# Performance work log

Hardware: AMD Instinct MI355X
Metric: run time of the kernel (lower is better)

## Reference

```python
import jax, jax.numpy as jnp
import numpy as np

D = 1024
H = 16
T_BLOCK = 2048


def setup_inputs() -> dict:
    key = jax.random.key(0)
    ks = jax.random.split(key, 12)
    B, T = 2, 2048
    s = lambda k, shape: jax.random.normal(k, shape, jnp.float32) * 0.02
    return {
        "x": jax.random.normal(ks[0], (B, T, D), jnp.float32),
        # layernorms
        "ln1_g": jnp.ones((D,), jnp.float32), "ln1_b": jnp.zeros((D,), jnp.float32),
        "ln2_g": jnp.ones((D,), jnp.float32), "ln2_b": jnp.zeros((D,), jnp.float32),
        # attention qkv projection ([in,out] layout) and output proj
        "w_qkv": s(ks[1], (D, 3 * D)), "b_qkv": jnp.zeros((3 * D,), jnp.float32),
        "w_o": s(ks[2], (D, D)), "b_o": jnp.zeros((D,), jnp.float32),
        # MLP
        "w_fc1": s(ks[3], (D, 4 * D)), "b_fc1": jnp.zeros((4 * D,), jnp.float32),
        "w_fc2": s(ks[4], (4 * D, D)), "b_fc2": jnp.zeros((D,), jnp.float32),
    }


def _layernorm(x, g, b, eps=1e-5):
    mu = jnp.mean(x, axis=-1, keepdims=True)
    var = jnp.var(x, axis=-1, keepdims=True)
    return (x - mu) * jax.lax.rsqrt(var + eps) * g + b


def _attention(x, w_qkv, b_qkv, w_o, b_o):
    B, T, C = x.shape
    hd = C // H
    qkv = x @ w_qkv + b_qkv                      # [B,T,3C]
    q, k, v = jnp.split(qkv, 3, axis=-1)
    split = lambda t: t.reshape(B, T, H, hd).transpose(0, 2, 1, 3)  # [B,H,T,hd]
    q, k, v = split(q), split(k), split(v)
    att = jnp.einsum("bhqd,bhkd->bhqk", q, k) / jnp.sqrt(jnp.float32(hd))
    causal = jnp.tril(jnp.ones((T, T), bool))
    att = jnp.where(causal[None, None], att, -jnp.inf)
    att = jax.nn.softmax(att, axis=-1)
    y = jnp.einsum("bhqk,bhkd->bhqd", att, v)    # [B,H,T,hd]
    y = y.transpose(0, 2, 1, 3).reshape(B, T, C)
    return y @ w_o + b_o


def reference(x, ln1_g, ln1_b, ln2_g, ln2_b, w_qkv, b_qkv, w_o, b_o,
              w_fc1, b_fc1, w_fc2, b_fc2):
    # dropout is identity in eval mode
    x = x + _attention(_layernorm(x, ln1_g, ln1_b), w_qkv, b_qkv, w_o, b_o)
    h = jax.nn.gelu(_layernorm(x, ln2_g, ln2_b) @ w_fc1 + b_fc1)
    return x + (h @ w_fc2 + b_fc2)
```

## Files before the change

kernel.cpp:

```cpp
#include <hip/hip_runtime.h>
#include <hip/hip_bf16.h>


using bf16 = __bf16;
using bf16x8 = __attribute__((ext_vector_type(8))) __bf16;
using floatx4 = __attribute__((ext_vector_type(4))) float;

#define D_ 1024
#define T_ 2048
#define B_ 2
#define H_ 16

static __device__ __forceinline__ bf16 f2bf(float f) { return (bf16)f; }

static __device__ __forceinline__ void async16(const void* g, void* l) {
  __builtin_amdgcn_global_load_lds(
      (const __attribute__((address_space(1))) void*)g,
      (__attribute__((address_space(3))) void*)l, 16, 0, 0);
}

static __device__ __forceinline__ float gelu_f(float v) {
  const float u2 = 1.5957691216057308f * (v + 0.044715f * v * v * v);
  return v / (1.0f + __expf(-u2));
}

static __device__ __forceinline__ void ln_row(const float* __restrict__ x,
                                              const float* __restrict__ g,
                                              const float* __restrict__ bsh,
                                              bf16* __restrict__ out,
                                              int row, int tid, float* red) {
  const float4 v = ((const float4*)(x + (size_t)row * D_))[tid];
  float s = v.x + v.y + v.z + v.w;
  float s2 = v.x * v.x + v.y * v.y + v.z * v.z + v.w * v.w;
  for (int off = 32; off; off >>= 1) {
    s += __shfl_xor(s, off);
    s2 += __shfl_xor(s2, off);
  }
  const int wave = tid >> 6, lane = tid & 63;
  if (lane == 0) { red[wave] = s; red[wave + 4] = s2; }
  __syncthreads();
  s = red[0] + red[1] + red[2] + red[3];
  s2 = red[4] + red[5] + red[6] + red[7];
  const float mu = s * (1.0f / D_);
  const float rstd = rsqrtf(s2 * (1.0f / D_) - mu * mu + 1e-5f);
  const float4 gv = ((const float4*)g)[tid];
  const float4 bv = ((const float4*)bsh)[tid];
  bf16 o[4] __attribute__((aligned(8)));
  o[0] = f2bf((v.x - mu) * rstd * gv.x + bv.x);
  o[1] = f2bf((v.y - mu) * rstd * gv.y + bv.y);
  o[2] = f2bf((v.z - mu) * rstd * gv.z + bv.z);
  o[3] = f2bf((v.w - mu) * rstd * gv.w + bv.w);
  *(ushort4*)(out + (size_t)row * D_ + tid * 4) = *(const ushort4*)o;
}

__global__ void transpose_cast_all(const float* __restrict__ w_qkv,
                                   const float* __restrict__ w_o,
                                   const float* __restrict__ w_fc1,
                                   const float* __restrict__ w_fc2,
                                   bf16* __restrict__ wqkvT, bf16* __restrict__ woT,
                                   bf16* __restrict__ wfc1T, bf16* __restrict__ wfc2T,
                                   const float* __restrict__ x,
                                   const float* __restrict__ ln1_g,
                                   const float* __restrict__ ln1_b,
                                   bf16* __restrict__ ln1) {
  int t = blockIdx.x;
  __shared__ float tile[32][33];
  if (t >= 12288) {
    const int tid = threadIdx.y * 32 + threadIdx.x;
    ln_row(x, ln1_g, ln1_b, ln1, t - 12288, tid, &tile[0][0]);
    return;
  }
  const float* in;
  bf16* out;
  int K, N, nx;
  if (t < 3072)      { in = w_qkv; out = wqkvT; K = 1024; N = 3072; nx = 96;  }
  else if (t < 4096) { in = w_o;   out = woT;   K = 1024; N = 1024; nx = 32;  t -= 3072; }
  else if (t < 8192) { in = w_fc1; out = wfc1T; K = 1024; N = 4096; nx = 128; t -= 4096; }
  else               { in = w_fc2; out = wfc2T; K = 4096; N = 1024; nx = 32;  t -= 8192; }
  const int n0 = (t % nx) * 32, k0 = (t / nx) * 32;
  const int tx = threadIdx.x, ty = threadIdx.y;
  for (int i = 0; i < 32; i += 8)
    tile[ty + i][tx] = in[(size_t)(k0 + ty + i) * N + n0 + tx];
  __syncthreads();
  for (int i = 0; i < 32; i += 8)
    out[(size_t)(n0 + ty + i) * K + k0 + tx] = f2bf(tile[tx][ty + i]);
}

__global__ __launch_bounds__(256)
void ln_kernel(const float* __restrict__ x, const float* __restrict__ g,
               const float* __restrict__ bsh, bf16* __restrict__ out) {
  __shared__ float red[8];
  ln_row(x, g, bsh, out, blockIdx.x, threadIdx.x, red);
}

template <int EPI>
__global__ __launch_bounds__(256)
void gemm_bt_sb(const bf16* __restrict__ A, const bf16* __restrict__ Bt,
                const float* __restrict__ bias, const float* __restrict__ res,
                void* __restrict__ Cout, int M, int N, int K) {
  __shared__ __align__(16) bf16 As[128][64];
  __shared__ __align__(16) bf16 Bs[128][64];
  const int tid = threadIdx.x;
  const int wave = tid >> 6, lane = tid & 63;
  const int quad = lane >> 4, l16 = lane & 15;
  const int wr = wave >> 1, wc = wave & 1;
  const int bm = blockIdx.x * 128, bn = blockIdx.y * 128;
  const int lrow8 = lane >> 3;
  const int lcol = (((lane & 7) ^ lrow8) * 8);

  floatx4 acc[4][4] = {};

  for (int k0 = 0; k0 < K; k0 += 64) {
    __syncthreads();
    for (int c = 0; c < 4; c++) {
      const int r = wave * 32 + c * 8;
      async16(&A[(size_t)(bm + r + lrow8) * K + k0 + lcol], &As[r][0]);
      async16(&Bt[(size_t)(bn + r + lrow8) * K + k0 + lcol], &Bs[r][0]);
    }
    __syncthreads();
    for (int ks = 0; ks < 2; ks++) {
      const int fc = ((quad + ks * 4) ^ (l16 & 7)) * 8;
      bf16x8 af[4], bfr[4];
      for (int mt = 0; mt < 4; mt++)
        af[mt] = *(const bf16x8*)&As[wr * 64 + mt * 16 + l16][fc];
      for (int nt = 0; nt < 4; nt++)
        bfr[nt] = *(const bf16x8*)&Bs[wc * 64 + nt * 16 + l16][fc];
      for (int mt = 0; mt < 4; mt++)
        for (int nt = 0; nt < 4; nt++)
          acc[mt][nt] = __builtin_amdgcn_mfma_f32_16x16x32_bf16(
              af[mt], bfr[nt], acc[mt][nt], 0, 0, 0);
    }
  }

  for (int mt = 0; mt < 4; mt++) {
    for (int nt = 0; nt < 4; nt++) {
      const int col = bn + wc * 64 + nt * 16 + l16;
      const float bcol = bias[col];
      for (int i = 0; i < 4; i++) {
        const int row = bm + wr * 64 + mt * 16 + quad * 4 + i;
        float v = acc[mt][nt][i] + bcol;
        if (EPI == 0) {
          ((bf16*)Cout)[(size_t)row * N + col] = f2bf(v);
        } else if (EPI == 1) {
          ((bf16*)Cout)[(size_t)row * N + col] = f2bf(gelu_f(v));
        } else {
          ((float*)Cout)[(size_t)row * N + col] = v + res[(size_t)row * N + col];
        }
      }
    }
  }
}

template <int EPI>
__global__ __launch_bounds__(256)
void gemm_bt(const bf16* __restrict__ A, const bf16* __restrict__ Bt,
             const float* __restrict__ bias, const float* __restrict__ res,
             void* __restrict__ Cout, int M, int N, int K) {
  __shared__ __align__(16) bf16 As[2][128][64];
  __shared__ __align__(16) bf16 Bs[2][128][64];
  const int tid = threadIdx.x;
  const int wave = tid >> 6, lane = tid & 63;
  const int quad = lane >> 4, l16 = lane & 15;
  const int wr = wave >> 1, wc = wave & 1;
  const int bm = blockIdx.x * 128, bn = blockIdx.y * 128;
  const int lrow8 = lane >> 3;
  const int lcol = (((lane & 7) ^ lrow8) * 8);

  const bf16* aBase = &A[(size_t)(bm + wave * 32 + lrow8) * K + lcol];
  const bf16* bBase = &Bt[(size_t)(bn + wave * 32 + lrow8) * K + lcol];

  auto stage = [&](int buf, int kk) {
    const int k0 = kk * 64;
    for (int c = 0; c < 4; c++) {
      async16(aBase + (size_t)c * 8 * K + k0, &As[buf][wave * 32 + c * 8][0]);
      async16(bBase + (size_t)c * 8 * K + k0, &Bs[buf][wave * 32 + c * 8][0]);
    }
  };

  floatx4 acc[4][4] = {};
  const int nsteps = K >> 6;

  stage(0, 0);
  if (nsteps > 1) stage(1, 1);
  int cur = 0;
  for (int t = 0; t < nsteps; ++t) {
    if (t < nsteps - 1)
      asm volatile("s_waitcnt vmcnt(8)" ::: "memory");
    else
      asm volatile("s_waitcnt vmcnt(0)" ::: "memory");
    __builtin_amdgcn_s_barrier();
    __builtin_amdgcn_sched_barrier(0);
    for (int ks = 0; ks < 2; ks++) {
      const int fc = ((quad + ks * 4) ^ (l16 & 7)) * 8;
      bf16x8 af[4], bfr[4];
      for (int mt = 0; mt < 4; mt++)
        af[mt] = *(const bf16x8*)&As[cur][wr * 64 + mt * 16 + l16][fc];
      for (int nn = 0; nn < 4; nn++)
        bfr[nn] = *(const bf16x8*)&Bs[cur][wc * 64 + nn * 16 + l16][fc];
      for (int mt = 0; mt < 4; mt++)
        for (int nn = 0; nn < 4; nn++)
          acc[mt][nn] = __builtin_amdgcn_mfma_f32_16x16x32_bf16(
              af[mt], bfr[nn], acc[mt][nn], 0, 0, 0);
    }
    __builtin_amdgcn_sched_barrier(0);
    __builtin_amdgcn_s_barrier();
    if (t + 2 < nsteps) stage(cur, t + 2);
    cur ^= 1;
  }

  for (int mt = 0; mt < 4; mt++) {
    for (int nn = 0; nn < 4; nn++) {
      const int col = bn + wc * 64 + nn * 16 + l16;
      const float bcol = bias[col];
      for (int i = 0; i < 4; i++) {
        const int row = bm + wr * 64 + mt * 16 + quad * 4 + i;
        float v = acc[mt][nn][i] + bcol;
        if (EPI == 0) {
          ((bf16*)Cout)[(size_t)row * N + col] = f2bf(v);
        } else if (EPI == 1) {
          ((bf16*)Cout)[(size_t)row * N + col] = f2bf(gelu_f(v));
        } else {
          ((float*)Cout)[(size_t)row * N + col] = v + res[(size_t)row * N + col];
        }
      }
    }
  }
}

template <int EPI>
__global__ __launch_bounds__(256)
void gemm64_k128(const bf16* __restrict__ A, const bf16* __restrict__ Bt,
                 const float* __restrict__ bias, const float* __restrict__ res,
                 void* __restrict__ Cout, int M, int N, int K) {
  __shared__ __align__(16) bf16 As[64][128];
  __shared__ __align__(16) bf16 Bs[128][128];
  const int tid = threadIdx.x;
  const int wave = tid >> 6, lane = tid & 63;
  const int quad = lane >> 4, l16 = lane & 15;
  const int wr = wave >> 1, wc = wave & 1;
  const int bm = blockIdx.x * 64, bn = blockIdx.y * 128;
  const int sr = lane >> 4;
  const int pchunk = lane & 15;

  floatx4 acc[2][4] = {};

  for (int k0 = 0; k0 < K; k0 += 128) {
    __syncthreads();
    for (int c = 0; c < 4; c++) {
      const int base = wave * 16 + c * 4;
      const int scol = (pchunk ^ ((c * 4 + sr) & 15)) * 8;
      async16(&A[(size_t)(bm + base + sr) * K + k0 + scol], &As[base][0]);
    }
    for (int c = 0; c < 8; c++) {
      const int base = wave * 32 + c * 4;
      const int scol = (pchunk ^ ((c * 4 + sr) & 15)) * 8;
      async16(&Bt[(size_t)(bn + base + sr) * K + k0 + scol], &Bs[base][0]);
    }
    __syncthreads();
    for (int ks = 0; ks < 4; ks++) {
      const int fc = ((quad + ks * 4) ^ l16) * 8;
      bf16x8 af[2], bfr[4];
      for (int mt = 0; mt < 2; mt++)
        af[mt] = *(const bf16x8*)&As[wr * 32 + mt * 16 + l16][fc];
      for (int nt = 0; nt < 4; nt++)
        bfr[nt] = *(const bf16x8*)&Bs[wc * 64 + nt * 16 + l16][fc];
      for (int mt = 0; mt < 2; mt++)
        for (int nt = 0; nt < 4; nt++)
          acc[mt][nt] = __builtin_amdgcn_mfma_f32_16x16x32_bf16(
              af[mt], bfr[nt], acc[mt][nt], 0, 0, 0);
    }
  }

  for (int mt = 0; mt < 2; mt++) {
    for (int nt = 0; nt < 4; nt++) {
      const int col = bn + wc * 64 + nt * 16 + l16;
      const float bcol = bias[col];
      for (int i = 0; i < 4; i++) {
        const int row = bm + wr * 32 + mt * 16 + quad * 4 + i;
        float v = acc[mt][nt][i] + bcol;
        if (EPI == 0) {
          ((bf16*)Cout)[(size_t)row * N + col] = f2bf(v);
        } else if (EPI == 1) {
          ((bf16*)Cout)[(size_t)row * N + col] = f2bf(gelu_f(v));
        } else {
          ((float*)Cout)[(size_t)row * N + col] = v + res[(size_t)row * N + col];
        }
      }
    }
  }
}

__global__ __launch_bounds__(512)
void attn_kernel(const bf16* __restrict__ qkv, bf16* __restrict__ y) {
  const int bh = blockIdx.y, b = bh >> 4, h = bh & 15;
  const int tile = (blockIdx.y & 16) ? (int)blockIdx.x : (15 - (int)blockIdx.x);
  const int q0 = tile * 128;
  const int tid = threadIdx.x, wave = tid >> 6, lane = tid & 63;
  const int quad = lane >> 4, l16 = lane & 15;
  const int l7 = l16 & 7;
  const int w16 = wave * 16;

  __shared__ __align__(16) bf16 Ks[64][64];
  __shared__ __align__(16) bf16 Vts[64][64];
  __shared__ __align__(16) bf16 Ps[128][64];

  const size_t bbase = (size_t)b * T_ * 3072 + (size_t)h * 64;
  const bf16* Qg = qkv + bbase;
  const bf16* Kg = qkv + bbase + 1024;
  const bf16* Vg = qkv + bbase + 2048;

  bf16x8 ones;
  for (int j = 0; j < 8; j++) ones[j] = f2bf(1.0f);

  const int kr = tid >> 3, kch = tid & 7;
  const int kcol = ((kch ^ (kr & 7)) * 8);
  const int vk = tid & 63, vd = tid >> 6;

  bf16x8 qf[2];
  for (int ks = 0; ks < 2; ks++) {
    bf16x8 t = *(const bf16x8*)
        &Qg[(size_t)(q0 + w16 + l16) * 3072 + ks * 32 + quad * 8];
    for (int j = 0; j < 8; j++) t[j] = f2bf((float)t[j] * 0.125f);
    qf[ks] = t;
  }

  int4 kreg = *(const int4*)&Kg[(size_t)kr * 3072 + kch * 8];
  bf16x8 vreg = *(const bf16x8*)&Vg[(size_t)vk * 3072 + vd * 8];

  floatx4 accY[4] = {};
  floatx4 accL = {};

  const int kend = q0 + 64;
  for (int kc = 0; kc <= kend; kc += 64) {
    __syncthreads();
    *(int4*)&Ks[kr][kcol] = kreg;
    for (int j = 0; j < 8; j++) {
      const int d = vd * 8 + j;
      Vts[d][((vk >> 3) ^ j) * 8 + (vk & 7)] = vreg[j];
    }
    __syncthreads();

    if (kc < kend) {
      kreg = *(const int4*)&Kg[(size_t)(kc + 64 + kr) * 3072 + kch * 8];
      vreg = *(const bf16x8*)&Vg[(size_t)(kc + 64 + vk) * 3072 + vd * 8];
    }

    floatx4 s[4];
    for (int nt = 0; nt < 4; nt++) {
      const bf16* krow = &Ks[nt * 16 + l16][0];
      bf16x8 kf0 = *(const bf16x8*)&krow[(quad ^ l7) * 8];
      bf16x8 kf1 = *(const bf16x8*)&krow[((4 + quad) ^ l7) * 8];
      floatx4 t = {};
      t = __builtin_amdgcn_mfma_f32_16x16x32_bf16(qf[0], kf0, t, 0, 0, 0);
      t = __builtin_amdgcn_mfma_f32_16x16x32_bf16(qf[1], kf1, t, 0, 0, 0);
      s[nt] = t;
    }
    if (kc + 64 > q0 + w16) {
      for (int nt = 0; nt < 4; nt++)
        for (int i = 0; i < 4; i++) {
          const int c = kc + nt * 16 + l16;
          const int r = q0 + w16 + quad * 4 + i;
          if (c > r) s[nt][i] = -1e30f;
        }
    }

    for (int i = 0; i < 4; i++) {
      const int pr = quad * 4 + i;
      bf16* prow = &Ps[w16 + pr][0];
      for (int nt = 0; nt < 4; nt++)
        prow[(((nt * 2 + (l16 >> 3)) ^ (pr & 7)) * 8) + l7] =
            f2bf(__expf(s[nt][i] - 8.0f));
    }
    __builtin_amdgcn_wave_barrier();

    for (int ks = 0; ks < 2; ks++) {
      bf16x8 pa = *(const bf16x8*)&Ps[w16 + l16][((ks * 4 + quad) ^ l7) * 8];
      for (int dt = 0; dt < 4; dt++) {
        bf16x8 vb = *(const bf16x8*)&Vts[dt * 16 + l16][((ks * 4 + quad) ^ l7) * 8];
        accY[dt] =
            __builtin_amdgcn_mfma_f32_16x16x32_bf16(pa, vb, accY[dt], 0, 0, 0);
      }
      accL = __builtin_amdgcn_mfma_f32_16x16x32_bf16(pa, ones, accL, 0, 0, 0);
    }
  }

  for (int i = 0; i < 4; i++) {
    const float linv = 1.0f / accL[i];
    const int r = q0 + w16 + quad * 4 + i;
    for (int dt = 0; dt < 4; dt++)
      y[(size_t)(b * T_ + r) * D_ + h * 64 + dt * 16 + l16] =
          f2bf(accY[dt][i] * linv);
  }
}

extern "C" void kernel_launch(void* const* d_in, const int* in_sizes, int n_in,
                              void* d_out, int out_size, void* d_ws, size_t ws_size,
                              hipStream_t stream) {
  const float* x     = (const float*)d_in[0];
  const float* ln1_g = (const float*)d_in[1];
  const float* ln1_b = (const float*)d_in[2];
  const float* ln2_g = (const float*)d_in[3];
  const float* ln2_b = (const float*)d_in[4];
  const float* w_qkv = (const float*)d_in[5];
  const float* b_qkv = (const float*)d_in[6];
  const float* w_o   = (const float*)d_in[7];
  const float* b_o   = (const float*)d_in[8];
  const float* w_fc1 = (const float*)d_in[9];
  const float* b_fc1 = (const float*)d_in[10];
  const float* w_fc2 = (const float*)d_in[11];
  const float* b_fc2 = (const float*)d_in[12];

  char* p = (char*)d_ws;
  bf16* wqkvT = (bf16*)p; p += (size_t)3072 * 1024 * 2;
  bf16* woT   = (bf16*)p; p += (size_t)1024 * 1024 * 2;
  bf16* wfc1T = (bf16*)p; p += (size_t)4096 * 1024 * 2;
  bf16* wfc2T = (bf16*)p; p += (size_t)1024 * 4096 * 2;
  bf16* ln1   = (bf16*)p; p += (size_t)4096 * 1024 * 2;
  bf16* qkv   = (bf16*)p; p += (size_t)4096 * 3072 * 2;
  bf16* yb    = (bf16*)p; p += (size_t)4096 * 1024 * 2;
  float* x2   = (float*)p; p += (size_t)4096 * 1024 * 4;
  bf16* ln2   = (bf16*)p; p += (size_t)4096 * 1024 * 2;
  bf16* hb    = (bf16*)p; p += (size_t)4096 * 4096 * 2;

  transpose_cast_all<<<dim3(16384), dim3(32, 8), 0, stream>>>(
      w_qkv, w_o, w_fc1, w_fc2, wqkvT, woT, wfc1T, wfc2T,
      x, ln1_g, ln1_b, ln1);

  gemm_bt_sb<0><<<dim3(32, 24), 256, 0, stream>>>(ln1, wqkvT, b_qkv, nullptr, qkv,
                                                  4096, 3072, 1024);
  attn_kernel<<<dim3(16, 32), 512, 0, stream>>>(qkv, yb);
  gemm64_k128<2><<<dim3(64, 8), 256, 0, stream>>>(yb, woT, b_o, x, x2,
                                                  4096, 1024, 1024);
  ln_kernel<<<4096, 256, 0, stream>>>(x2, ln2_g, ln2_b, ln2);
  gemm_bt<1><<<dim3(32, 32), 256, 0, stream>>>(ln2, wfc1T, b_fc1, nullptr, hb,
                                               4096, 4096, 1024);
  gemm64_k128<2><<<dim3(64, 8), 256, 0, stream>>>(hb, wfc2T, b_fc2, x2, (float*)d_out,
                                                  4096, 1024, 4096);
}
```

Before: 305.1 us.

## Use 256x256 tile, 8-wave GEMM for the FC1 GELU projection

Replaces the 128x128, 4-wave FC1 GEMM with a 256x256-tile kernel using 512 threads in a 2x4 wave grid. Each wave now computes a 128x64 output block and reuses its B fragments across two halves of A. The aim is higher arithmetic intensity per LDS and global load, and the grid shrinks to 256 blocks, about one per CU. It also adds s_setprio around the MFMA bursts and fully unrolls the loops. In exchange, the doubled tile needs 128KB of LDS and twice the accumulator registers, which limits occupancy to one block per CU and leaves no second wave of blocks to cover latency.

Result: no change. 304.4 us (-0.2%).

```diff
diff --git a/kernel.cpp b/kernel.cpp
--- a/kernel.cpp
+++ b/kernel.cpp
@@ -152,17 +152,17 @@
 }
 
 template <int EPI>
-__global__ __launch_bounds__(256)
-void gemm_bt(const bf16* __restrict__ A, const bf16* __restrict__ Bt,
-             const float* __restrict__ bias, const float* __restrict__ res,
-             void* __restrict__ Cout, int M, int N, int K) {
-  __shared__ __align__(16) bf16 As[2][128][64];
-  __shared__ __align__(16) bf16 Bs[2][128][64];
+__global__ __launch_bounds__(512, 2)
+void gemm256u(const bf16* __restrict__ A, const bf16* __restrict__ Bt,
+              const float* __restrict__ bias, const float* __restrict__ res,
+              void* __restrict__ Cout, int M, int N, int K) {
+  __shared__ __align__(16) bf16 As[2][256][64];
+  __shared__ __align__(16) bf16 Bs[2][256][64];
   const int tid = threadIdx.x;
   const int wave = tid >> 6, lane = tid & 63;
   const int quad = lane >> 4, l16 = lane & 15;
-  const int wr = wave >> 1, wc = wave & 1;
-  const int bm = blockIdx.x * 128, bn = blockIdx.y * 128;
+  const int wr = wave >> 2, wc = wave & 3;
+  const int bm = blockIdx.x * 256, bn = blockIdx.y * 256;
   const int lrow8 = lane >> 3;
   const int lcol = (((lane & 7) ^ lrow8) * 8);
 
@@ -171,13 +171,14 @@
 
   auto stage = [&](int buf, int kk) {
     const int k0 = kk * 64;
+#pragma unroll
     for (int c = 0; c < 4; c++) {
       async16(aBase + (size_t)c * 8 * K + k0, &As[buf][wave * 32 + c * 8][0]);
       async16(bBase + (size_t)c * 8 * K + k0, &Bs[buf][wave * 32 + c * 8][0]);
     }
   };
 
-  floatx4 acc[4][4] = {};
+  floatx4 acc[8][4] = {};
   const int nsteps = K >> 6;
 
   stage(0, 0);
@@ -190,17 +191,29 @@
       asm volatile("s_waitcnt vmcnt(0)" ::: "memory");
     __builtin_amdgcn_s_barrier();
     __builtin_amdgcn_sched_barrier(0);
+#pragma unroll
     for (int ks = 0; ks < 2; ks++) {
       const int fc = ((quad + ks * 4) ^ (l16 & 7)) * 8;
-      bf16x8 af[4], bfr[4];
-      for (int mt = 0; mt < 4; mt++)
-        af[mt] = *(const bf16x8*)&As[cur][wr * 64 + mt * 16 + l16][fc];
-      for (int nn = 0; nn < 4; nn++)
-        bfr[nn] = *(const bf16x8*)&Bs[cur][wc * 64 + nn * 16 + l16][fc];
-      for (int mt = 0; mt < 4; mt++)
-        for (int nn = 0; nn < 4; nn++)
-          acc[mt][nn] = __builtin_amdgcn_mfma_f32_16x16x32_bf16(
-              af[mt], bfr[nn], acc[mt][nn], 0, 0, 0);
+      bf16x8 bfr[4];
+#pragma unroll
+      for (int nt = 0; nt < 4; nt++)
+        bfr[nt] = *(const bf16x8*)&Bs[cur][wc * 64 + nt * 16 + l16][fc];
+#pragma unroll
+      for (int half = 0; half < 2; half++) {
+        bf16x8 af[4];
+#pragma unroll
+        for (int m = 0; m < 4; m++)
+          af[m] = *(const bf16x8*)
+              &As[cur][wr * 128 + (half * 4 + m) * 16 + l16][fc];
+        __builtin_amdgcn_s_setprio(1);
+#pragma unroll
+        for (int m = 0; m < 4; m++)
+#pragma unroll
+          for (int nt = 0; nt < 4; nt++)
+            acc[half * 4 + m][nt] = __builtin_amdgcn_mfma_f32_16x16x32_bf16(
+                af[m], bfr[nt], acc[half * 4 + m][nt], 0, 0, 0);
+        __builtin_amdgcn_s_setprio(0);
+      }
     }
     __builtin_amdgcn_sched_barrier(0);
     __builtin_amdgcn_s_barrier();
@@ -208,13 +221,16 @@
     cur ^= 1;
   }
 
-  for (int mt = 0; mt < 4; mt++) {
-    for (int nn = 0; nn < 4; nn++) {
-      const int col = bn + wc * 64 + nn * 16 + l16;
+#pragma unroll
+  for (int mt = 0; mt < 8; mt++) {
+#pragma unroll
+    for (int nt = 0; nt < 4; nt++) {
+      const int col = bn + wc * 64 + nt * 16 + l16;
       const float bcol = bias[col];
+#pragma unroll
       for (int i = 0; i < 4; i++) {
-        const int row = bm + wr * 64 + mt * 16 + quad * 4 + i;
-        float v = acc[mt][nn][i] + bcol;
+        const int row = bm + wr * 128 + mt * 16 + quad * 4 + i;
+        float v = acc[mt][nt][i] + bcol;
         if (EPI == 0) {
           ((bf16*)Cout)[(size_t)row * N + col] = f2bf(v);
         } else if (EPI == 1) {
@@ -432,8 +448,8 @@
   gemm64_k128<2><<<dim3(64, 8), 256, 0, stream>>>(yb, woT, b_o, x, x2,
                                                   4096, 1024, 1024);
   ln_kernel<<<4096, 256, 0, stream>>>(x2, ln2_g, ln2_b, ln2);
-  gemm_bt<1><<<dim3(32, 32), 256, 0, stream>>>(ln2, wfc1T, b_fc1, nullptr, hb,
-                                               4096, 4096, 1024);
+  gemm256u<1><<<dim3(16, 16), 512, 0, stream>>>(ln2, wfc1T, b_fc1, nullptr, hb,
+                                                4096, 4096, 1024);
   gemm64_k128<2><<<dim3(64, 8), 256, 0, stream>>>(hb, wfc2T, b_fc2, x2, (float*)d_out,
                                                   4096, 1024, 4096);
 }
```
